# Kernel optimization log

Hardware: AMD Instinct MI355X
Metric: run time of the kernel (lower is better)

## Reference

```python
import jax, jax.numpy as jnp
import numpy as np

T, B, V, E, H, L = 70, 64, 10000, 512, 1024, 2


def setup_inputs() -> dict:
    key = jax.random.key(0)
    ks = jax.random.split(key, 10)
    k = float(1.0 / np.sqrt(H))
    u = lambda kk, shape, a: jax.random.uniform(kk, shape, jnp.float32, -a, a)
    return {
        "inputs": jax.random.randint(ks[0], (T, B), 0, V, dtype=jnp.int32),
        "hidden": jnp.zeros((L, B, H), jnp.float32),
        "emb_W": u(ks[1], (V, E), 0.1),
        "Wx0": u(ks[2], (H, E), k),   # nn.Linear weight is [out, in]
        "Wx1": u(ks[3], (H, H), k),
        "Wh0": u(ks[4], (H, H), k),
        "bh0": u(ks[5], (H,), k),
        "Wh1": u(ks[6], (H, H), k),
        "bh1": u(ks[7], (H,), k),
        "Wy": u(ks[8], (V, H), 0.1),
        "by": jnp.zeros((V,), jnp.float32),
    }


def reference(inputs, hidden, emb_W, Wx0, Wx1, Wh0, bh0, Wh1, bh1, Wy, by):
    # Stacked Elman RNN, dropout identity (dp_keep_prob=1.0).
    embedded = emb_W[inputs]  # [T, B, E]

    def step(h, x_t):
        # h: [L, B, H]; x_t: [B, E]
        h0 = jnp.tanh(x_t @ Wx0.T + h[0] @ Wh0.T + bh0)
        h1 = jnp.tanh(h0 @ Wx1.T + h[1] @ Wh1.T + bh1)
        new_h = jnp.stack([h0, h1])  # [L, B, H]
        logits_t = h1 @ Wy.T + by    # [B, V]
        return new_h, logits_t

    h_final, logits = jax.lax.scan(step, hidden, embedded)
    return logits, h_final  # [T, B, V], [L, B, H]
```

## Files before the change

### kernel.cpp

```cpp
#include <hip/hip_runtime.h>
#include <hip/hip_bf16.h>
#include <cmath>
#include <cstdint>


using u16 = unsigned short;
using u32 = unsigned int;
using u64 = unsigned long long;
typedef __attribute__((ext_vector_type(8))) short short8;
typedef __attribute__((ext_vector_type(4))) float f32x4;

#define MFMA_BF16(a, b, c) __builtin_amdgcn_mfma_f32_16x16x32_bf16((a), (b), (c), 0, 0, 0)

__device__ __forceinline__ u16 bf16_rne(float x) {
    u32 u = __float_as_uint(x);
    u32 r = u + 0x7FFFu + ((u >> 16) & 1u);
    return (u16)(r >> 16);
}
__device__ __forceinline__ float bf16_f(u16 h) {
    return __uint_as_float(((u32)h) << 16);
}
__device__ __forceinline__ void split2(float x, u16& hi, u16& lo) {
    hi = bf16_rne(x);
    lo = bf16_rne(x - bf16_f(hi));
}
__device__ __forceinline__ u64 pack4(u16 a, u16 b, u16 c, u16 d) {
    return (u64)a | ((u64)b << 16) | ((u64)c << 32) | ((u64)d << 48);
}

__device__ __forceinline__ void wait_count(int* f, int target) {
    if (threadIdx.x == 0) {
        while (__hip_atomic_load(f, __ATOMIC_RELAXED, __HIP_MEMORY_SCOPE_AGENT) < target)
            __builtin_amdgcn_s_sleep(16);
    }
    __syncthreads();
}
__device__ __forceinline__ void wait_count2(int* f0, int tgt0, int* f1, int tgt1) {
    if (threadIdx.x == 0) {
        for (;;) {
            int v0 = __hip_atomic_load(f0, __ATOMIC_RELAXED, __HIP_MEMORY_SCOPE_AGENT);
            int v1 = __hip_atomic_load(f1, __ATOMIC_RELAXED, __HIP_MEMORY_SCOPE_AGENT);
            if (v0 >= tgt0 && v1 >= tgt1) break;
            __builtin_amdgcn_s_sleep(16);
        }
    }
    __syncthreads();
}
__device__ __forceinline__ void signal_done(int* f) {
    __syncthreads();
    if (threadIdx.x == 0)
        __hip_atomic_fetch_add(f, 1, __ATOMIC_RELAXED, __HIP_MEMORY_SCOPE_AGENT);
}

__global__ __launch_bounds__(256) void split_kernel(
    const float* __restrict__ src, u16* __restrict__ hi, u16* __restrict__ lo, int n4)
{
    int g = blockIdx.x * 256 + threadIdx.x;
    if (g >= n4) return;
    float4 v = *reinterpret_cast<const float4*>(src + (size_t)g * 4);
    u16 h0,h1,h2,h3,l0,l1,l2,l3;
    split2(v.x,h0,l0); split2(v.y,h1,l1); split2(v.z,h2,l2); split2(v.w,h3,l3);
    ushort4 H = {h0,h1,h2,h3}, L = {l0,l1,l2,l3};
    *reinterpret_cast<ushort4*>(hi + (size_t)g * 4) = H;
    *reinterpret_cast<ushort4*>(lo + (size_t)g * 4) = L;
}

__global__ __launch_bounds__(256) void gather_split_kernel(
    const float* __restrict__ emb, const int* __restrict__ idx,
    u16* __restrict__ hi, u16* __restrict__ lo, int n4)
{
    int g = blockIdx.x * 256 + threadIdx.x;
    if (g >= n4) return;
    int m  = g >> 7;
    int c4 = g & 127;
    const float* src = emb + (size_t)idx[m] * 512 + c4 * 4;
    float4 v = *reinterpret_cast<const float4*>(src);
    u16 h0,h1,h2,h3,l0,l1,l2,l3;
    split2(v.x,h0,l0); split2(v.y,h1,l1); split2(v.z,h2,l2); split2(v.w,h3,l3);
    ushort4 H = {h0,h1,h2,h3}, L = {l0,l1,l2,l3};
    size_t o = (size_t)m * 512 + c4 * 4;
    *reinterpret_cast<ushort4*>(hi + o) = H;
    *reinterpret_cast<ushort4*>(lo + o) = L;
}

__device__ __forceinline__ void gemm_tile(
    const u16* __restrict__ Ah, const u16* __restrict__ Al,
    const u16* __restrict__ Bh, const u16* __restrict__ Bl,
    const float* __restrict__ bias, float* __restrict__ C,
    int N, int K, int m0, int n0,
    u16* sAh, u16* sAl, u16* sBh, u16* sBl)
{
    const int tid  = threadIdx.x;
    const int lane = tid & 63;
    const int w    = tid >> 6;
    const int wr   = w >> 1, wc = w & 1;

    f32x4 acc[4][4];
    #pragma unroll
    for (int i = 0; i < 4; ++i)
        #pragma unroll
        for (int j = 0; j < 4; ++j) acc[i][j] = 0.0f;

    for (int k0 = 0; k0 < K; k0 += 32) {
        #pragma unroll
        for (int r = 0; r < 2; ++r) {
            int s   = r * 256 + tid;
            int row = s >> 2, q = s & 3;
            int gq  = q ^ (row & 3);
            int l16 = row * 32 + q * 8;
            size_t ga = (size_t)(m0 + row) * K + k0 + gq * 8;
            int brow = n0 + row; if (brow >= N) brow = N - 1;
            size_t gb = (size_t)brow * K + k0 + gq * 8;
            *reinterpret_cast<int4*>(sAh + l16) = *reinterpret_cast<const int4*>(Ah + ga);
            *reinterpret_cast<int4*>(sAl + l16) = *reinterpret_cast<const int4*>(Al + ga);
            *reinterpret_cast<int4*>(sBh + l16) = *reinterpret_cast<const int4*>(Bh + gb);
            *reinterpret_cast<int4*>(sBl + l16) = *reinterpret_cast<const int4*>(Bl + gb);
        }
        __syncthreads();

        const int q4 = lane >> 4;
        short8 afh[4], afl[4];
        #pragma unroll
        for (int i = 0; i < 4; ++i) {
            int ra  = wr * 64 + i * 16 + (lane & 15);
            int off = ra * 32 + (q4 ^ (ra & 3)) * 8;
            afh[i] = *reinterpret_cast<const short8*>(sAh + off);
            afl[i] = *reinterpret_cast<const short8*>(sAl + off);
        }
        #pragma unroll
        for (int j = 0; j < 4; ++j) {
            int rb  = wc * 64 + j * 16 + (lane & 15);
            int off = rb * 32 + (q4 ^ (rb & 3)) * 8;
            short8 bfh = *reinterpret_cast<const short8*>(sBh + off);
            short8 bfl = *reinterpret_cast<const short8*>(sBl + off);
            #pragma unroll
            for (int i = 0; i < 4; ++i) {
                acc[i][j] = MFMA_BF16(afh[i], bfh, acc[i][j]);
                acc[i][j] = MFMA_BF16(afh[i], bfl, acc[i][j]);
                acc[i][j] = MFMA_BF16(afl[i], bfh, acc[i][j]);
            }
        }
        __syncthreads();
    }

    #pragma unroll
    for (int j = 0; j < 4; ++j) {
        int n = n0 + wc * 64 + j * 16 + (lane & 15);
        if (n < N) {
            float bv = bias[n];
            #pragma unroll
            for (int i = 0; i < 4; ++i) {
                #pragma unroll
                for (int r = 0; r < 4; ++r) {
                    int m = m0 + wr * 64 + i * 16 + (lane >> 4) * 4 + r;
                    C[(size_t)m * N + n] = acc[i][j][r] + bv;
                }
            }
        }
    }
}

__global__ __launch_bounds__(256) void gemm_mfma(
    const u16* __restrict__ Ah, const u16* __restrict__ Al,
    const u16* __restrict__ Bh, const u16* __restrict__ Bl,
    const float* __restrict__ bias, float* __restrict__ C,
    int M, int N, int K)
{
    __shared__ u16 sAh[128*32], sAl[128*32], sBh[128*32], sBl[128*32];
    gemm_tile(Ah, Al, Bh, Bl, bias, C, N, K,
              blockIdx.y * 128, blockIdx.x * 128, sAh, sAl, sBh, sBl);
}

__global__ __launch_bounds__(256) void gemm_mfma_swz(
    const u16* __restrict__ Ah, const u16* __restrict__ Al,
    const u16* __restrict__ Bh, const u16* __restrict__ Bl,
    const float* __restrict__ bias, float* __restrict__ C,
    int M, int N, int K)
{
    __shared__ u16 sAh[128*32], sAl[128*32], sBh[128*32], sBl[128*32];
    const int NTN = 79;
    const int nwg = 35 * 79;
    const int q = nwg / 8, r = nwg % 8;
    int orig = (int)blockIdx.x;
    int xcd  = orig % 8;
    int idx  = orig / 8;
    int wg   = (xcd < r) ? (xcd * (q + 1) + idx)
                         : (r * (q + 1) + (xcd - r) * q + idx);
    int mb = wg / NTN, nb = wg % NTN;
    gemm_tile(Ah, Al, Bh, Bl, bias, C, N, K,
              mb * 128, nb * 128, sAh, sAl, sBh, sBl);
}

__global__ __launch_bounds__(256, 1) void rnn_persist2(
    const float* __restrict__ A0,
    const u16* __restrict__ hs0h, const u16* __restrict__ hs0l,
    const u16* __restrict__ hs1h, const u16* __restrict__ hs1l,
    u16* __restrict__ H0h, u16* __restrict__ H0l,
    u16* __restrict__ H1h, u16* __restrict__ H1l,
    const u16* __restrict__ Wh0h, const u16* __restrict__ Wh0l,
    const u16* __restrict__ Wx1h, const u16* __restrict__ Wx1l,
    const u16* __restrict__ Wh1h, const u16* __restrict__ Wh1l,
    const float* __restrict__ bh1, int* flags)
{
    __shared__ u16 sW[65536];
    __shared__ float sStage[64 * 17];
    const int tid   = threadIdx.x;
    const int lane  = tid & 63;
    const int w     = tid >> 6;
    const int layer = blockIdx.x >> 6;
    const int n0    = (int)(blockIdx.x & 63) * 16;
    const int m0    = w * 16;
    const int rb    = lane & 15;
    const int q4    = lane >> 4;
    const int arow  = m0 + rb;
    const size_t BH = 65536;
    const int srow  = tid >> 2;
    const int sc4   = (tid & 3) * 4;

    if (layer == 0) {
        for (int i = 0; i < 16; ++i) {
            int s    = i * 256 + tid;
            int arr  = s >> 11;
            int r    = (s >> 7) & 15;
            int g    = s & 127;
            int slot = g ^ (r & 7);
            const u16* src = (arr ? Wh0l : Wh0h) + (size_t)(n0 + r) * 1024 + g * 8;
            *reinterpret_cast<int4*>(sW + arr * 16384 + r * 1024 + slot * 8) =
                *reinterpret_cast<const int4*>(src);
        }
    } else {
        for (int i = 0; i < 32; ++i) {
            int s    = i * 256 + tid;
            int arr  = s >> 12;
            int r    = (s >> 8) & 15;
            int g    = s & 255;
            int slot = g ^ (r & 7);
            const u16* src;
            if (g < 128) src = (arr ? Wx1l : Wx1h) + (size_t)(n0 + r) * 1024 + g * 8;
            else         src = (arr ? Wh1l : Wh1h) + (size_t)(n0 + r) * 1024 + (g - 128) * 8;
            *reinterpret_cast<int4*>(sW + arr * 32768 + r * 2048 + slot * 8) =
                *reinterpret_cast<const int4*>(src);
        }
    }
    __syncthreads();

    if (layer == 0) {
        for (int t = 0; t < 70; ++t) {
            if (t > 0) wait_count(flags + (t - 1), 64);
            const u16* hph = t ? H0h + (size_t)(t - 1) * BH : hs0h;
            const u16* hpl = t ? H0l + (size_t)(t - 1) * BH : hs0l;
            f32x4 acc = {0.f, 0.f, 0.f, 0.f};
            #pragma unroll 8
            for (int kt = 0; kt < 32; ++kt) {
                short8 ah = *reinterpret_cast<const short8*>(hph + (size_t)arow * 1024 + kt * 32 + q4 * 8);
                short8 al = *reinterpret_cast<const short8*>(hpl + (size_t)arow * 1024 + kt * 32 + q4 * 8);
                int slot = (kt * 4 + q4) ^ (rb & 7);
                short8 bh = *reinterpret_cast<const short8*>(sW + rb * 1024 + slot * 8);
                short8 bl = *reinterpret_cast<const short8*>(sW + 16384 + rb * 1024 + slot * 8);
                acc = MFMA_BF16(ah, bh, acc);
                acc = MFMA_BF16(ah, bl, acc);
                acc = MFMA_BF16(al, bh, acc);
            }
            #pragma unroll
            for (int r = 0; r < 4; ++r) {
                int m = m0 + q4 * 4 + r;
                size_t o = (size_t)t * BH + (size_t)m * 1024 + n0 + rb;
                sStage[m * 17 + rb] = tanhf(acc[r] + A0[o]);
            }
            __syncthreads();
            {
                float f0 = sStage[srow * 17 + sc4 + 0];
                float f1 = sStage[srow * 17 + sc4 + 1];
                float f2 = sStage[srow * 17 + sc4 + 2];
                float f3 = sStage[srow * 17 + sc4 + 3];
                u16 a,b,c,d, la,lb,lc,ld;
                split2(f0,a,la); split2(f1,b,lb); split2(f2,c,lc); split2(f3,d,ld);
                size_t o64 = ((size_t)t * BH + (size_t)srow * 1024 + n0 + sc4) >> 2;
                __hip_atomic_store((u64*)H0h + o64, pack4(a,b,c,d),
                                   __ATOMIC_RELAXED, __HIP_MEMORY_SCOPE_AGENT);
                __hip_atomic_store((u64*)H0l + o64, pack4(la,lb,lc,ld),
                                   __ATOMIC_RELAXED, __HIP_MEMORY_SCOPE_AGENT);
            }
            signal_done(flags + t);
        }
    } else {
        for (int t = 0; t < 70; ++t) {
            if (t > 0) wait_count2(flags + t, 64, flags + 70 + (t - 1), 64);
            else       wait_count(flags + t, 64);
            const u16* h0h  = H0h + (size_t)t * BH;
            const u16* h0l  = H0l + (size_t)t * BH;
            const u16* h1ph = t ? H1h + (size_t)(t - 1) * BH : hs1h;
            const u16* h1pl = t ? H1l + (size_t)(t - 1) * BH : hs1l;
            f32x4 acc = {0.f, 0.f, 0.f, 0.f};
            #pragma unroll 8
            for (int kt = 0; kt < 32; ++kt) {
                short8 ah = *reinterpret_cast<const short8*>(h0h + (size_t)arow * 1024 + kt * 32 + q4 * 8);
                short8 al = *reinterpret_cast<const short8*>(h0l + (size_t)arow * 1024 + kt * 32 + q4 * 8);
                int slot = (kt * 4 + q4) ^ (rb & 7);
                short8 bh = *reinterpret_cast<const short8*>(sW + rb * 2048 + slot * 8);
                short8 bl = *reinterpret_cast<const short8*>(sW + 32768 + rb * 2048 + slot * 8);
                acc = MFMA_BF16(ah, bh, acc);
                acc = MFMA_BF16(ah, bl, acc);
                acc = MFMA_BF16(al, bh, acc);
            }
            #pragma unroll 8
            for (int kt = 32; kt < 64; ++kt) {
                int ko = (kt - 32) * 32;
                short8 ah = *reinterpret_cast<const short8*>(h1ph + (size_t)arow * 1024 + ko + q4 * 8);
                short8 al = *reinterpret_cast<const short8*>(h1pl + (size_t)arow * 1024 + ko + q4 * 8);
                int slot = (kt * 4 + q4) ^ (rb & 7);
                short8 bh = *reinterpret_cast<const short8*>(sW + rb * 2048 + slot * 8);
                short8 bl = *reinterpret_cast<const short8*>(sW + 32768 + rb * 2048 + slot * 8);
                acc = MFMA_BF16(ah, bh, acc);
                acc = MFMA_BF16(ah, bl, acc);
                acc = MFMA_BF16(al, bh, acc);
            }
            const int n = n0 + rb;
            #pragma unroll
            for (int r = 0; r < 4; ++r) {
                int m = m0 + q4 * 4 + r;
                sStage[m * 17 + rb] = tanhf(acc[r] + bh1[n]);
            }
            __syncthreads();
            {
                float f0 = sStage[srow * 17 + sc4 + 0];
                float f1 = sStage[srow * 17 + sc4 + 1];
                float f2 = sStage[srow * 17 + sc4 + 2];
                float f3 = sStage[srow * 17 + sc4 + 3];
                u16 a,b,c,d, la,lb,lc,ld;
                split2(f0,a,la); split2(f1,b,lb); split2(f2,c,lc); split2(f3,d,ld);
                size_t o64 = ((size_t)t * BH + (size_t)srow * 1024 + n0 + sc4) >> 2;
                __hip_atomic_store((u64*)H1h + o64, pack4(a,b,c,d),
                                   __ATOMIC_RELAXED, __HIP_MEMORY_SCOPE_AGENT);
                __hip_atomic_store((u64*)H1l + o64, pack4(la,lb,lc,ld),
                                   __ATOMIC_RELAXED, __HIP_MEMORY_SCOPE_AGENT);
            }
            signal_done(flags + 70 + t);
        }
    }
}

__global__ __launch_bounds__(256) void hfinal_kernel(
    const u16* __restrict__ H0h, const u16* __restrict__ H0l,
    const u16* __restrict__ H1h, const u16* __restrict__ H1l,
    float* __restrict__ outp)
{
    int i = blockIdx.x * 256 + threadIdx.x;
    outp[i]         = bf16_f(H0h[i]) + bf16_f(H0l[i]);
    outp[65536 + i] = bf16_f(H1h[i]) + bf16_f(H1l[i]);
}

extern "C" void kernel_launch(void* const* d_in, const int* in_sizes, int n_in,
                              void* d_out, int out_size, void* d_ws, size_t ws_size,
                              hipStream_t stream)
{
    const int*   inputs = (const int*)  d_in[0];
    const float* hidden = (const float*)d_in[1];
    const float* embW   = (const float*)d_in[2];
    const float* Wx0    = (const float*)d_in[3];
    const float* Wx1    = (const float*)d_in[4];
    const float* Wh0    = (const float*)d_in[5];
    const float* bh0    = (const float*)d_in[6];
    const float* Wh1    = (const float*)d_in[7];
    const float* bh1    = (const float*)d_in[8];
    const float* Wy     = (const float*)d_in[9];
    const float* by     = (const float*)d_in[10];
    float* out = (float*)d_out;

    const int T = 70, B = 64, V = 10000, E = 512, H = 1024;
    const int M = T * B;
    const size_t MH = (size_t)M * H;
    const size_t BH = (size_t)B * H;

    char* wsb = (char*)d_ws;
    u16*   Wyh  = (u16*)(wsb);
    u16*   Wyl  = Wyh + (size_t)V * H;
    float* buf0 = (float*)(wsb + 40960000);
    u16*   H0h  = (u16*)(wsb + 59310080);
    u16*   H0l  = H0h + MH;
    u16*   H1h  = H0l + MH;
    u16*   H1l  = H1h + MH;
    u16*   Wx0h = H1l + MH;
    u16*   Wx0l = Wx0h + (size_t)H * E;
    u16*   Wx1h = Wx0l + (size_t)H * E;
    u16*   Wx1l = Wx1h + (size_t)H * H;
    u16*   Wh0h = Wx1l + (size_t)H * H;
    u16*   Wh0l = Wh0h + (size_t)H * H;
    u16*   Wh1h = Wh0l + (size_t)H * H;
    u16*   Wh1l = Wh1h + (size_t)H * H;
    u16*   hs0h = Wh1l + (size_t)H * H;
    u16*   hs0l = hs0h + BH;
    u16*   hs1h = hs0l + BH;
    u16*   hs1l = hs1h + BH;

    u16*   Agh   = (u16*)((char*)d_out + 20971520);
    u16*   Agl   = Agh + (size_t)M * E;
    int*   flags = (int*)((char*)d_out + 104857600);

    dim3 blk(256);

    hipMemsetAsync(flags, 0, 140 * sizeof(int), stream);

    split_kernel<<<dim3((H*E)/1024), blk, 0, stream>>>(Wx0, Wx0h, Wx0l, (H*E)/4);
    split_kernel<<<dim3((H*H)/1024), blk, 0, stream>>>(Wx1, Wx1h, Wx1l, (H*H)/4);
    split_kernel<<<dim3((H*H)/1024), blk, 0, stream>>>(Wh0, Wh0h, Wh0l, (H*H)/4);
    split_kernel<<<dim3((H*H)/1024), blk, 0, stream>>>(Wh1, Wh1h, Wh1l, (H*H)/4);
    split_kernel<<<dim3((V*H)/1024), blk, 0, stream>>>(Wy,  Wyh,  Wyl,  (V*H)/4);
    split_kernel<<<dim3(64), blk, 0, stream>>>(hidden,      hs0h, hs0l, (int)BH/4);
    split_kernel<<<dim3(64), blk, 0, stream>>>(hidden + BH, hs1h, hs1l, (int)BH/4);
    gather_split_kernel<<<dim3((M*E)/1024), blk, 0, stream>>>(embW, inputs, Agh, Agl, (M*E)/4);

    gemm_mfma<<<dim3(H/128, M/128), blk, 0, stream>>>(
        Agh, Agl, Wx0h, Wx0l, bh0, buf0, M, H, E);

    {
        const float* A0p = buf0;
        void* args[] = {
            (void*)&A0p,
            (void*)&hs0h, (void*)&hs0l, (void*)&hs1h, (void*)&hs1l,
            (void*)&H0h,  (void*)&H0l,  (void*)&H1h,  (void*)&H1l,
            (void*)&Wh0h, (void*)&Wh0l, (void*)&Wx1h, (void*)&Wx1l,
            (void*)&Wh1h, (void*)&Wh1l, (void*)&bh1, (void*)&flags
        };
        hipLaunchCooperativeKernel(reinterpret_cast<void*>(rnn_persist2),
                                   dim3(128), blk, args, 0, stream);
    }

    hfinal_kernel<<<dim3(256), blk, 0, stream>>>(
        H0h + (size_t)(T-1) * BH, H0l + (size_t)(T-1) * BH,
        H1h + (size_t)(T-1) * BH, H1l + (size_t)(T-1) * BH,
        out + (size_t)M * V);

    gemm_mfma_swz<<<dim3(35 * 79), blk, 0, stream>>>(
        H1h, H1l, Wyh, Wyl, by, out, M, V, H);
}
```

Baseline: 1.560 ms.

## Widen persistent RNN blocks to 32 columns, stream low weights from global

The persistent recurrence kernel now uses 64 workgroups of 512 threads instead of 128 of 256. Each workgroup computes a 64x32 output tile, so the flag barriers wait on 32 producers rather than 64. Only the high bf16 weight halves are kept in LDS; the low halves are read straight from global/L2 inside the MFMA loop. The K loop is split across four independent accumulators to add MFMA-level parallelism, and the hi/lo split now happens before staging. The aim is to cut per-step synchronization and raise per-wave ILP, at the cost of extra global traffic for the low weights and fewer CUs in use.

```diff
diff --git a/kernel.cpp b/kernel.cpp
--- a/kernel.cpp
+++ b/kernel.cpp
@@ -191,7 +191,29 @@
               mb * 128, nb * 128, sAh, sAl, sBh, sBl);
 }
 
-__global__ __launch_bounds__(256, 1) void rnn_persist2(
+#define L0C(accv, ktv) { \
+    int kt_ = (ktv); \
+    short8 ah_ = *reinterpret_cast<const short8*>(hph + (size_t)arow * 1024 + kt_ * 32 + q4 * 8); \
+    short8 al_ = *reinterpret_cast<const short8*>(hpl + (size_t)arow * 1024 + kt_ * 32 + q4 * 8); \
+    int slot_ = (kt_ * 4 + q4) ^ (cl & 7); \
+    short8 bh_ = *reinterpret_cast<const short8*>(sW + cl * 1024 + slot_ * 8); \
+    short8 bl_ = *reinterpret_cast<const short8*>(Wh0l + (size_t)(n0 + cl) * 1024 + kt_ * 32 + q4 * 8); \
+    accv = MFMA_BF16(ah_, bh_, accv); \
+    accv = MFMA_BF16(ah_, bl_, accv); \
+    accv = MFMA_BF16(al_, bh_, accv); }
+
+#define L1C(accv, ktv, sbase, ph, pl, BlPtr) { \
+    int kt_ = (ktv); \
+    short8 ah_ = *reinterpret_cast<const short8*>((ph) + (size_t)arow * 1024 + kt_ * 32 + q4 * 8); \
+    short8 al_ = *reinterpret_cast<const short8*>((pl) + (size_t)arow * 1024 + kt_ * 32 + q4 * 8); \
+    int slot_ = (((sbase) + kt_) * 4 + q4) ^ (cl & 7); \
+    short8 bh_ = *reinterpret_cast<const short8*>(sW + cl * 2048 + slot_ * 8); \
+    short8 bl_ = *reinterpret_cast<const short8*>((BlPtr) + (size_t)(n0 + cl) * 1024 + kt_ * 32 + q4 * 8); \
+    accv = MFMA_BF16(ah_, bh_, accv); \
+    accv = MFMA_BF16(ah_, bl_, accv); \
+    accv = MFMA_BF16(al_, bh_, accv); }
+
+__global__ __launch_bounds__(512, 1) void rnn_persist4(
     const float* __restrict__ A0,
     const u16* __restrict__ hs0h, const u16* __restrict__ hs0l,
     const u16* __restrict__ hs1h, const u16* __restrict__ hs1l,
@@ -203,42 +225,43 @@
     const float* __restrict__ bh1, int* flags)
 {
     __shared__ u16 sW[65536];
-    __shared__ float sStage[64 * 17];
+    __shared__ u16 sStageH[64 * 36];
+    __shared__ u16 sStageL[64 * 36];
     const int tid   = threadIdx.x;
     const int lane  = tid & 63;
     const int w     = tid >> 6;
-    const int layer = blockIdx.x >> 6;
-    const int n0    = (int)(blockIdx.x & 63) * 16;
-    const int m0    = w * 16;
+    const int wr    = w >> 1;
+    const int wc    = w & 1;
+    const int layer = (int)(blockIdx.x >> 5);
+    const int bidx  = (int)(blockIdx.x & 31);
+    const int n0    = bidx * 32;
     const int rb    = lane & 15;
     const int q4    = lane >> 4;
-    const int arow  = m0 + rb;
+    const int arow  = wr * 16 + rb;
+    const int cl    = wc * 16 + rb;
     const size_t BH = 65536;
-    const int srow  = tid >> 2;
-    const int sc4   = (tid & 3) * 4;
+    const int srow  = tid >> 3;
+    const int sc4   = (tid & 7) * 4;
 
     if (layer == 0) {
+        for (int i = 0; i < 8; ++i) {
+            int s    = i * 512 + tid;
+            int c    = s >> 7;
+            int g    = s & 127;
+            int slot = g ^ (c & 7);
+            *reinterpret_cast<int4*>(sW + c * 1024 + slot * 8) =
+                *reinterpret_cast<const int4*>(Wh0h + (size_t)(n0 + c) * 1024 + g * 8);
+        }
+    } else {
         for (int i = 0; i < 16; ++i) {
-            int s    = i * 256 + tid;
-            int arr  = s >> 11;
-            int r    = (s >> 7) & 15;
-            int g    = s & 127;
-            int slot = g ^ (r & 7);
-            const u16* src = (arr ? Wh0l : Wh0h) + (size_t)(n0 + r) * 1024 + g * 8;
-            *reinterpret_cast<int4*>(sW + arr * 16384 + r * 1024 + slot * 8) =
-                *reinterpret_cast<const int4*>(src);
-        }
-    } else {
-        for (int i = 0; i < 32; ++i) {
-            int s    = i * 256 + tid;
-            int arr  = s >> 12;
-            int r    = (s >> 8) & 15;
+            int s    = i * 512 + tid;
+            int c    = s >> 8;
             int g    = s & 255;
-            int slot = g ^ (r & 7);
-            const u16* src;
-            if (g < 128) src = (arr ? Wx1l : Wx1h) + (size_t)(n0 + r) * 1024 + g * 8;
-            else         src = (arr ? Wh1l : Wh1h) + (size_t)(n0 + r) * 1024 + (g - 128) * 8;
-            *reinterpret_cast<int4*>(sW + arr * 32768 + r * 2048 + slot * 8) =
+            int slot = g ^ (c & 7);
+            const u16* src = (g < 128)
+                ? Wx1h + (size_t)(n0 + c) * 1024 + g * 8
+                : Wh1h + (size_t)(n0 + c) * 1024 + (g - 128) * 8;
+            *reinterpret_cast<int4*>(sW + c * 2048 + slot * 8) =
                 *reinterpret_cast<const int4*>(src);
         }
     }
@@ -246,93 +269,75 @@
 
     if (layer == 0) {
         for (int t = 0; t < 70; ++t) {
-            if (t > 0) wait_count(flags + (t - 1), 64);
+            if (t > 0) wait_count(flags + (t - 1), 32);
             const u16* hph = t ? H0h + (size_t)(t - 1) * BH : hs0h;
             const u16* hpl = t ? H0l + (size_t)(t - 1) * BH : hs0l;
-            f32x4 acc = {0.f, 0.f, 0.f, 0.f};
-            #pragma unroll 8
-            for (int kt = 0; kt < 32; ++kt) {
-                short8 ah = *reinterpret_cast<const short8*>(hph + (size_t)arow * 1024 + kt * 32 + q4 * 8);
-                short8 al = *reinterpret_cast<const short8*>(hpl + (size_t)arow * 1024 + kt * 32 + q4 * 8);
-                int slot = (kt * 4 + q4) ^ (rb & 7);
-                short8 bh = *reinterpret_cast<const short8*>(sW + rb * 1024 + slot * 8);
-                short8 bl = *reinterpret_cast<const short8*>(sW + 16384 + rb * 1024 + slot * 8);
-                acc = MFMA_BF16(ah, bh, acc);
-                acc = MFMA_BF16(ah, bl, acc);
-                acc = MFMA_BF16(al, bh, acc);
-            }
+            f32x4 c0 = {0.f,0.f,0.f,0.f}, c1 = {0.f,0.f,0.f,0.f};
+            f32x4 c2 = {0.f,0.f,0.f,0.f}, c3 = {0.f,0.f,0.f,0.f};
+            #pragma unroll
+            for (int i = 0; i < 8; ++i) {
+                L0C(c0, i);
+                L0C(c1, 8 + i);
+                L0C(c2, 16 + i);
+                L0C(c3, 24 + i);
+            }
+            f32x4 acc = (c0 + c1) + (c2 + c3);
             #pragma unroll
             for (int r = 0; r < 4; ++r) {
-                int m = m0 + q4 * 4 + r;
-                size_t o = (size_t)t * BH + (size_t)m * 1024 + n0 + rb;
-                sStage[m * 17 + rb] = tanhf(acc[r] + A0[o]);
+                int m = wr * 16 + q4 * 4 + r;
+                size_t o = (size_t)t * BH + (size_t)m * 1024 + n0 + cl;
+                float hv = tanhf(acc[r] + A0[o]);
+                u16 hi, lo; split2(hv, hi, lo);
+                sStageH[m * 36 + cl] = hi;
+                sStageL[m * 36 + cl] = lo;
             }
             __syncthreads();
             {
-                float f0 = sStage[srow * 17 + sc4 + 0];
-                float f1 = sStage[srow * 17 + sc4 + 1];
-                float f2 = sStage[srow * 17 + sc4 + 2];
-                float f3 = sStage[srow * 17 + sc4 + 3];
-                u16 a,b,c,d, la,lb,lc,ld;
-                split2(f0,a,la); split2(f1,b,lb); split2(f2,c,lc); split2(f3,d,ld);
+                ushort4 hv = *reinterpret_cast<const ushort4*>(sStageH + srow * 36 + sc4);
+                ushort4 lv = *reinterpret_cast<const ushort4*>(sStageL + srow * 36 + sc4);
                 size_t o64 = ((size_t)t * BH + (size_t)srow * 1024 + n0 + sc4) >> 2;
-                __hip_atomic_store((u64*)H0h + o64, pack4(a,b,c,d),
+                __hip_atomic_store((u64*)H0h + o64, pack4(hv.x,hv.y,hv.z,hv.w),
                                    __ATOMIC_RELAXED, __HIP_MEMORY_SCOPE_AGENT);
-                __hip_atomic_store((u64*)H0l + o64, pack4(la,lb,lc,ld),
+                __hip_atomic_store((u64*)H0l + o64, pack4(lv.x,lv.y,lv.z,lv.w),
                                    __ATOMIC_RELAXED, __HIP_MEMORY_SCOPE_AGENT);
             }
             signal_done(flags + t);
         }
     } else {
         for (int t = 0; t < 70; ++t) {
-            if (t > 0) wait_count2(flags + t, 64, flags + 70 + (t - 1), 64);
-            else       wait_count(flags + t, 64);
+            if (t > 0) wait_count2(flags + t, 32, flags + 70 + (t - 1), 32);
+            else       wait_count(flags + t, 32);
             const u16* h0h  = H0h + (size_t)t * BH;
             const u16* h0l  = H0l + (size_t)t * BH;
             const u16* h1ph = t ? H1h + (size_t)(t - 1) * BH : hs1h;
             const u16* h1pl = t ? H1l + (size_t)(t - 1) * BH : hs1l;
-            f32x4 acc = {0.f, 0.f, 0.f, 0.f};
-            #pragma unroll 8
-            for (int kt = 0; kt < 32; ++kt) {
-                short8 ah = *reinterpret_cast<const short8*>(h0h + (size_t)arow * 1024 + kt * 32 + q4 * 8);
-                short8 al = *reinterpret_cast<const short8*>(h0l + (size_t)arow * 1024 + kt * 32 + q4 * 8);
-                int slot = (kt * 4 + q4) ^ (rb & 7);
-                short8 bh = *reinterpret_cast<const short8*>(sW + rb * 2048 + slot * 8);
-                short8 bl = *reinterpret_cast<const short8*>(sW + 32768 + rb * 2048 + slot * 8);
-                acc = MFMA_BF16(ah, bh, acc);
-                acc = MFMA_BF16(ah, bl, acc);
-                acc = MFMA_BF16(al, bh, acc);
-            }
-            #pragma unroll 8
-            for (int kt = 32; kt < 64; ++kt) {
-                int ko = (kt - 32) * 32;
-                short8 ah = *reinterpret_cast<const short8*>(h1ph + (size_t)arow * 1024 + ko + q4 * 8);
-                short8 al = *reinterpret_cast<const short8*>(h1pl + (size_t)arow * 1024 + ko + q4 * 8);
-                int slot = (kt * 4 + q4) ^ (rb & 7);
-                short8 bh = *reinterpret_cast<const short8*>(sW + rb * 2048 + slot * 8);
-                short8 bl = *reinterpret_cast<const short8*>(sW + 32768 + rb * 2048 + slot * 8);
-                acc = MFMA_BF16(ah, bh, acc);
-                acc = MFMA_BF16(ah, bl, acc);
-                acc = MFMA_BF16(al, bh, acc);
-            }
-            const int n = n0 + rb;
+            f32x4 c0 = {0.f,0.f,0.f,0.f}, c1 = {0.f,0.f,0.f,0.f};
+            f32x4 c2 = {0.f,0.f,0.f,0.f}, c3 = {0.f,0.f,0.f,0.f};
+            #pragma unroll
+            for (int i = 0; i < 16; ++i) {
+                L1C(c0, i,       0,  h0h,  h0l,  Wx1l);
+                L1C(c1, 16 + i,  0,  h0h,  h0l,  Wx1l);
+                L1C(c2, i,       32, h1ph, h1pl, Wh1l);
+                L1C(c3, 16 + i,  32, h1ph, h1pl, Wh1l);
+            }
+            f32x4 acc = (c0 + c1) + (c2 + c3);
+            const int n = n0 + cl;
             #pragma unroll
             for (int r = 0; r < 4; ++r) {
-                int m = m0 + q4 * 4 + r;
-                sStage[m * 17 + rb] = tanhf(acc[r] + bh1[n]);
+                int m = wr * 16 + q4 * 4 + r;
+                float hv = tanhf(acc[r] + bh1[n]);
+                u16 hi, lo; split2(hv, hi, lo);
+                sStageH[m * 36 + cl] = hi;
+                sStageL[m * 36 + cl] = lo;
             }
             __syncthreads();
             {
-                float f0 = sStage[srow * 17 + sc4 + 0];
-                float f1 = sStage[srow * 17 + sc4 + 1];
-                float f2 = sStage[srow * 17 + sc4 + 2];
-                float f3 = sStage[srow * 17 + sc4 + 3];
-                u16 a,b,c,d, la,lb,lc,ld;
-                split2(f0,a,la); split2(f1,b,lb); split2(f2,c,lc); split2(f3,d,ld);
+                ushort4 hv = *reinterpret_cast<const ushort4*>(sStageH + srow * 36 + sc4);
+                ushort4 lv = *reinterpret_cast<const ushort4*>(sStageL + srow * 36 + sc4);
                 size_t o64 = ((size_t)t * BH + (size_t)srow * 1024 + n0 + sc4) >> 2;
-                __hip_atomic_store((u64*)H1h + o64, pack4(a,b,c,d),
+                __hip_atomic_store((u64*)H1h + o64, pack4(hv.x,hv.y,hv.z,hv.w),
                                    __ATOMIC_RELAXED, __HIP_MEMORY_SCOPE_AGENT);
-                __hip_atomic_store((u64*)H1l + o64, pack4(la,lb,lc,ld),
+                __hip_atomic_store((u64*)H1l + o64, pack4(lv.x,lv.y,lv.z,lv.w),
                                    __ATOMIC_RELAXED, __HIP_MEMORY_SCOPE_AGENT);
             }
             signal_done(flags + 70 + t);
@@ -422,8 +427,8 @@
             (void*)&Wh0h, (void*)&Wh0l, (void*)&Wx1h, (void*)&Wx1l,
             (void*)&Wh1h, (void*)&Wh1l, (void*)&bh1, (void*)&flags
         };
-        hipLaunchCooperativeKernel(reinterpret_cast<void*>(rnn_persist2),
-                                   dim3(128), blk, args, 0, stream);
+        hipLaunchCooperativeKernel(reinterpret_cast<void*>(rnn_persist4),
+                                   dim3(64), dim3(512), args, 0, stream);
     }
 
     hfinal_kernel<<<dim3(256), blk, 0, stream>>>(
```

Measured after the change: 3.289 ms. 2.11x slower.
